# Kernel tuning notes

Measured on AMD Instinct MI355X. Metric: run time of the kernel, lower is better.

## Reference

```python
import jax, jax.numpy as jnp
import numpy as np


def setup_inputs() -> dict:
    key = jax.random.key(0)
    ks = jax.random.split(key, 6)
    B, H, N, C, O, G = 4, 24, 512, 120, 512, 5
    x = jax.random.normal(ks[0], (B, H, N, C), dtype=jnp.float32)
    t_indices = jnp.arange(H, dtype=jnp.int64)
    time_emb = jax.random.normal(ks[1], (H, 8), dtype=jnp.float32)
    # kaiming-uniform-ish init for base linear weight
    fan_in = C + 8
    bound = float(np.sqrt(6.0 / fan_in))
    base_w = jax.random.uniform(ks[2], (O, C + 8), minval=-bound, maxval=bound, dtype=jnp.float32)
    base_b = jax.random.uniform(ks[3], (O,), minval=-1.0 / np.sqrt(fan_in), maxval=1.0 / np.sqrt(fan_in), dtype=jnp.float32)
    spline_weight = jax.random.uniform(ks[4], (O, C + 8, G), minval=-0.1, maxval=0.1, dtype=jnp.float32)
    return {"x": x, "t_indices": t_indices, "time_emb": time_emb,
            "base_w": base_w, "base_b": base_b, "spline_weight": spline_weight}


def reference(x, t_indices, time_emb, base_w, base_b, spline_weight):
    B, H, N, C = x.shape
    G = spline_weight.shape[-1]
    grid = jnp.linspace(-1.0, 1.0, G, dtype=x.dtype)  # non-trainable buffer
    # time embedding lookup, broadcast over batch and nodes: [B,H,N,8]
    t_emb = jnp.broadcast_to(time_emb[t_indices][None, :, None, :], (B, H, N, time_emb.shape[-1]))
    x_in = jnp.concatenate([x, t_emb], axis=-1)  # [B,H,N,C+8]
    # base path: SiLU then linear
    base = jnp.einsum('bhni,oi->bhno', jax.nn.silu(x_in), base_w) + base_b
    # RBF basis: [B,H,N,C+8,G]
    inv_h = (G - 1) / 2.0  # 1 / (2/(G-1))
    basis = jnp.exp(-(((x_in[..., None] - grid) * inv_h) ** 2))
    spline = jnp.einsum('bhnig,oig->bhno', basis, spline_weight)
    return base + spline
```

## Files before the change

### kernel.cpp

```cpp
#include <hip/hip_runtime.h>
#include <hip/hip_bf16.h>

typedef __attribute__((ext_vector_type(4))) float f32x4;
typedef __attribute__((ext_vector_type(8))) short bf16x8;

#define GLDS16(gp, lp) __builtin_amdgcn_global_load_lds( \
    (__attribute__((address_space(1))) void*)(void*)(gp), \
    (__attribute__((address_space(3))) void*)(lp), 16, 0, 0)

static constexpr int Mtot = 49152;
static constexpr int Otot = 512;
static constexpr int Hh   = 24;

__device__ inline unsigned short f2bf(float f) {
    __hip_bfloat16 h = __float2bfloat16(f);
    unsigned short u;
    __builtin_memcpy(&u, &h, 2);
    return u;
}

__global__ __launch_bounds__(256) void prep_W(
        const float* __restrict__ bw, const float* __restrict__ sw,
        uint4* __restrict__ Wt)
{
    int tid = blockIdx.x * 256 + threadIdx.x;
    int p    = tid & 15;
    int o    = (tid >> 4) & 511;
    int iter = tid >> 13;
    int ck = p ^ (o & 7);
    unsigned u[4] = {0u, 0u, 0u, 0u};
    if (ck < 12) {
        unsigned short s[8];
        #pragma unroll
        for (int e = 0; e < 8; ++e) {
            int k = iter * 96 + ck * 8 + e;
            int i = k / 6, f = k - i * 6;
            float v = (f == 0) ? bw[o * 128 + i] : sw[(o * 128 + i) * 5 + (f - 1)];
            s[e] = f2bf(v);
        }
        #pragma unroll
        for (int n = 0; n < 4; ++n) u[n] = s[2 * n] | ((unsigned)s[2 * n + 1] << 16);
    }
    Wt[tid] = make_uint4(u[0], u[1], u[2], u[3]);
}

__global__ __launch_bounds__(256, 2) void gemm_kan(
        const float* __restrict__ x, const int* __restrict__ t_idx,
        const float* __restrict__ temb,
        const char* __restrict__ Wt,
        const float* __restrict__ bias,
        float* __restrict__ out)
{
    __shared__ char AsB[64 * 256];
    __shared__ char BsB[256 * 256];
    const int t    = threadIdx.x;
    const int wave = t >> 6;
    const int lane = t & 63;
    const int ll   = lane & 15;
    const int q4   = lane >> 4;
    const int wn   = wave * 64;
    const int m_base = blockIdx.y * 64;
    const int n_base = blockIdx.x * 256;

    f32x4 acc[4][4] = {};

    const char* bsrc0 = Wt + (size_t)(n_base + wn) * 256 + lane * 16;
    char* ldsB = BsB + wn * 256;

    const int row = t >> 2;
    const int q   = t & 3;
    const int ht  = t_idx[(m_base >> 9) % Hh];
    const float* xrow = x + (size_t)(m_base + row) * 120;
    const float* trow = temb + ht * 8;

    auto chanptr = [&](int i0) -> const float* {
        return (i0 < 120) ? (xrow + i0) : (trow + (i0 - 120));
    };

    float4 xv = *(const float4*)chanptr(4 * q);

    constexpr float C1 = 0.36787944117f;
    constexpr float C4 = 0.01831563889f;

    #pragma unroll
    for (int it = 0; it < 8; ++it) {
        const char* bsrc = bsrc0 + (size_t)it * (512 * 256);
        #pragma unroll
        for (int p = 0; p < 16; ++p)
            GLDS16(bsrc + p * 1024, ldsB + p * 1024);

        const float4 cur = xv;
        if (it < 7) xv = *(const float4*)chanptr((it + 1) * 16 + 4 * q);

        float v[4] = {cur.x, cur.y, cur.z, cur.w};
        unsigned short s[24];
        #pragma unroll
        for (int c = 0; c < 4; ++c) {
            const float vv = v[c];
            s[c * 6 + 0] = f2bf(vv * __builtin_amdgcn_rcpf(1.0f + __expf(-vv)));
            const float tt = __expf(-4.0f * vv * vv);
            const float uu = __expf(4.0f * vv);
            const float rr = __builtin_amdgcn_rcpf(uu);
            const float tu = tt * uu, tr = tt * rr;
            s[c * 6 + 1] = f2bf(tr * rr * C4);
            s[c * 6 + 2] = f2bf(tr * C1);
            s[c * 6 + 3] = f2bf(tt);
            s[c * 6 + 4] = f2bf(tu * C1);
            s[c * 6 + 5] = f2bf(tu * uu * C4);
        }
        #pragma unroll
        for (int j = 0; j < 3; ++j) {
            const int ck = 3 * q + j;
            const int phys = ck ^ (row & 7);
            unsigned u[4];
            #pragma unroll
            for (int n = 0; n < 4; ++n)
                u[n] = s[j * 8 + 2 * n] | ((unsigned)s[j * 8 + 2 * n + 1] << 16);
            *(uint4*)(AsB + row * 256 + phys * 16) = make_uint4(u[0], u[1], u[2], u[3]);
        }
        __syncthreads();

        #pragma unroll
        for (int kk = 0; kk < 3; ++kk) {
            bf16x8 af[4], bf[4];
            #pragma unroll
            for (int mi = 0; mi < 4; ++mi) {
                const int r = mi * 16 + ll;
                af[mi] = *(const bf16x8*)(AsB + r * 256 + (((kk * 4 + q4) ^ (ll & 7)) * 16));
            }
            #pragma unroll
            for (int ni = 0; ni < 4; ++ni) {
                const int r = wn + ni * 16 + ll;
                bf[ni] = *(const bf16x8*)(BsB + r * 256 + (((kk * 4 + q4) ^ (ll & 7)) * 16));
            }
            #pragma unroll
            for (int mi = 0; mi < 4; ++mi)
                #pragma unroll
                for (int ni = 0; ni < 4; ++ni)
                    acc[mi][ni] = __builtin_amdgcn_mfma_f32_16x16x32_bf16(
                        af[mi], bf[ni], acc[mi][ni], 0, 0, 0);
        }
        __syncthreads();
    }

    const int col0 = n_base + wn + ll;
    const int row0 = m_base + q4 * 4;
    #pragma unroll
    for (int ni = 0; ni < 4; ++ni) {
        const int col = col0 + ni * 16;
        const float bv = bias[col];
        #pragma unroll
        for (int mi = 0; mi < 4; ++mi) {
            #pragma unroll
            for (int r = 0; r < 4; ++r) {
                out[(long)(row0 + mi * 16 + r) * Otot + col] = acc[mi][ni][r] + bv;
            }
        }
    }
}

extern "C" void kernel_launch(void* const* d_in, const int* in_sizes, int n_in,
                              void* d_out, int out_size, void* d_ws, size_t ws_size,
                              hipStream_t stream) {
    const float* x    = (const float*)d_in[0];
    const int*   tidx = (const int*)  d_in[1];
    const float* temb = (const float*)d_in[2];
    const float* bw   = (const float*)d_in[3];
    const float* bb   = (const float*)d_in[4];
    const float* sw   = (const float*)d_in[5];
    float* out = (float*)d_out;

    char* Wt = (char*)d_ws;

    prep_W<<<65536 / 256, 256, 0, stream>>>(bw, sw, (uint4*)Wt);
    gemm_kan<<<dim3(Otot / 256, Mtot / 64), 256, 0, stream>>>(
        x, tidx, temb, Wt, bb, out);
}
```

Before: 171.1 us.

## Retile KAN GEMM to 128x128 blocks with chunk-major LDS and block swizzle

Changes the block tile from 64x256 to 128x128 with a 2x2 wave layout, so each block computes twice as many A-side basis rows and shares them across fewer B columns. The LDS layout becomes chunk-major (16-byte chunk by row) with no XOR swizzle, and the prepacked weights are laid out the same way, which also drops the padding chunks. LDS use falls from 80KB to 48KB, allowing 3 blocks per CU, and a grouped blockIdx swizzle is meant to improve L2 reuse. The aim is to cut redundant activation/basis computation and weight traffic per output. The risk is LDS bank conflicts from the unswizzled layout.

```diff
diff --git a/kernel.cpp b/kernel.cpp
--- a/kernel.cpp
+++ b/kernel.cpp
@@ -23,52 +23,51 @@
         const float* __restrict__ bw, const float* __restrict__ sw,
         uint4* __restrict__ Wt)
 {
-    int tid = blockIdx.x * 256 + threadIdx.x;
-    int p    = tid & 15;
-    int o    = (tid >> 4) & 511;
-    int iter = tid >> 13;
-    int ck = p ^ (o & 7);
-    unsigned u[4] = {0u, 0u, 0u, 0u};
-    if (ck < 12) {
-        unsigned short s[8];
-        #pragma unroll
-        for (int e = 0; e < 8; ++e) {
-            int k = iter * 96 + ck * 8 + e;
-            int i = k / 6, f = k - i * 6;
-            float v = (f == 0) ? bw[o * 128 + i] : sw[(o * 128 + i) * 5 + (f - 1)];
-            s[e] = f2bf(v);
-        }
-        #pragma unroll
-        for (int n = 0; n < 4; ++n) u[n] = s[2 * n] | ((unsigned)s[2 * n + 1] << 16);
+    const int tid = blockIdx.x * 256 + threadIdx.x;
+    const int col = tid & 511;
+    const int cc  = tid >> 9;
+    const int k0  = cc * 8;
+    unsigned short s[8];
+    #pragma unroll
+    for (int e = 0; e < 8; ++e) {
+        const int k = k0 + e;
+        const int i = k / 6, f = k - i * 6;
+        const float v = (f == 0) ? bw[col * 128 + i]
+                                 : sw[(col * 128 + i) * 5 + (f - 1)];
+        s[e] = f2bf(v);
     }
-    Wt[tid] = make_uint4(u[0], u[1], u[2], u[3]);
+    uint4 u;
+    u.x = s[0] | ((unsigned)s[1] << 16);
+    u.y = s[2] | ((unsigned)s[3] << 16);
+    u.z = s[4] | ((unsigned)s[5] << 16);
+    u.w = s[6] | ((unsigned)s[7] << 16);
+    Wt[tid] = u;
 }
 
-__global__ __launch_bounds__(256, 2) void gemm_kan(
+__global__ __launch_bounds__(256, 3) void gemm_kan(
         const float* __restrict__ x, const int* __restrict__ t_idx,
         const float* __restrict__ temb,
         const char* __restrict__ Wt,
         const float* __restrict__ bias,
         float* __restrict__ out)
 {
-    __shared__ char AsB[64 * 256];
-    __shared__ char BsB[256 * 256];
+    __shared__ char Alds[12 * 128 * 16];
+    __shared__ char Blds[12 * 128 * 16];
     const int t    = threadIdx.x;
     const int wave = t >> 6;
     const int lane = t & 63;
     const int ll   = lane & 15;
     const int q4   = lane >> 4;
-    const int wn   = wave * 64;
-    const int m_base = blockIdx.y * 64;
-    const int n_base = blockIdx.x * 256;
+    const int wm   = (wave >> 1) * 64;
+    const int wn   = (wave & 1) * 64;
 
-    f32x4 acc[4][4] = {};
+    const int bid = blockIdx.x;
+    const int swz = (bid & 7) * 192 + (bid >> 3);
+    const int m_base = (swz >> 2) * 128;
+    const int n_base = (swz & 3) * 128;
 
-    const char* bsrc0 = Wt + (size_t)(n_base + wn) * 256 + lane * 16;
-    char* ldsB = BsB + wn * 256;
-
-    const int row = t >> 2;
-    const int q   = t & 3;
+    const int row = t >> 1;
+    const int hh  = t & 1;
     const int ht  = t_idx[(m_base >> 9) % Hh];
     const float* xrow = x + (size_t)(m_base + row) * 120;
     const float* trow = temb + ht * 8;
@@ -77,25 +76,40 @@
         return (i0 < 120) ? (xrow + i0) : (trow + (i0 - 120));
     };
 
-    float4 xv = *(const float4*)chanptr(4 * q);
+    f32x4 acc[4][4] = {};
+
+    float4 xa, xb;
+    {
+        const float* p = chanptr(hh * 8);
+        xa = *(const float4*)p;
+        xb = *(const float4*)(p + 4);
+    }
 
     constexpr float C1 = 0.36787944117f;
     constexpr float C4 = 0.01831563889f;
 
     #pragma unroll
     for (int it = 0; it < 8; ++it) {
-        const char* bsrc = bsrc0 + (size_t)it * (512 * 256);
         #pragma unroll
-        for (int p = 0; p < 16; ++p)
-            GLDS16(bsrc + p * 1024, ldsB + p * 1024);
+        for (int j = 0; j < 6; ++j) {
+            const int c = wave * 3 + (j >> 1);
+            const int g = (j & 1) * 64;
+            const char* src = Wt + (((size_t)(it * 12 + c) * 512 + n_base + g) << 4)
+                              + lane * 16;
+            GLDS16(src, Blds + ((c * 128 + g) << 4));
+        }
 
-        const float4 cur = xv;
-        if (it < 7) xv = *(const float4*)chanptr((it + 1) * 16 + 4 * q);
+        const float4 ca = xa, cb = xb;
+        if (it < 7) {
+            const float* p = chanptr((it + 1) * 16 + hh * 8);
+            xa = *(const float4*)p;
+            xb = *(const float4*)(p + 4);
+        }
 
-        float v[4] = {cur.x, cur.y, cur.z, cur.w};
-        unsigned short s[24];
+        const float v[8] = {ca.x, ca.y, ca.z, ca.w, cb.x, cb.y, cb.z, cb.w};
+        unsigned short s[48];
         #pragma unroll
-        for (int c = 0; c < 4; ++c) {
+        for (int c = 0; c < 8; ++c) {
             const float vv = v[c];
             s[c * 6 + 0] = f2bf(vv * __builtin_amdgcn_rcpf(1.0f + __expf(-vv)));
             const float tt = __expf(-4.0f * vv * vv);
@@ -109,30 +123,26 @@
             s[c * 6 + 5] = f2bf(tu * uu * C4);
         }
         #pragma unroll
-        for (int j = 0; j < 3; ++j) {
-            const int ck = 3 * q + j;
-            const int phys = ck ^ (row & 7);
+        for (int j = 0; j < 6; ++j) {
+            const int ck = 6 * hh + j;
             unsigned u[4];
             #pragma unroll
             for (int n = 0; n < 4; ++n)
                 u[n] = s[j * 8 + 2 * n] | ((unsigned)s[j * 8 + 2 * n + 1] << 16);
-            *(uint4*)(AsB + row * 256 + phys * 16) = make_uint4(u[0], u[1], u[2], u[3]);
+            *(uint4*)(Alds + ((ck * 128 + row) << 4)) = make_uint4(u[0], u[1], u[2], u[3]);
         }
         __syncthreads();
 
         #pragma unroll
         for (int kk = 0; kk < 3; ++kk) {
+            const int ch = kk * 4 + q4;
             bf16x8 af[4], bf[4];
             #pragma unroll
-            for (int mi = 0; mi < 4; ++mi) {
-                const int r = mi * 16 + ll;
-                af[mi] = *(const bf16x8*)(AsB + r * 256 + (((kk * 4 + q4) ^ (ll & 7)) * 16));
-            }
+            for (int mi = 0; mi < 4; ++mi)
+                af[mi] = *(const bf16x8*)(Alds + ((ch * 128 + wm + mi * 16 + ll) << 4));
             #pragma unroll
-            for (int ni = 0; ni < 4; ++ni) {
-                const int r = wn + ni * 16 + ll;
-                bf[ni] = *(const bf16x8*)(BsB + r * 256 + (((kk * 4 + q4) ^ (ll & 7)) * 16));
-            }
+            for (int ni = 0; ni < 4; ++ni)
+                bf[ni] = *(const bf16x8*)(Blds + ((ch * 128 + wn + ni * 16 + ll) << 4));
             #pragma unroll
             for (int mi = 0; mi < 4; ++mi)
                 #pragma unroll
@@ -144,7 +154,7 @@
     }
 
     const int col0 = n_base + wn + ll;
-    const int row0 = m_base + q4 * 4;
+    const int row0 = m_base + wm + q4 * 4;
     #pragma unroll
     for (int ni = 0; ni < 4; ++ni) {
         const int col = col0 + ni * 16;
@@ -172,7 +182,6 @@
 
     char* Wt = (char*)d_ws;
 
-    prep_W<<<65536 / 256, 256, 0, stream>>>(bw, sw, (uint4*)Wt);
-    gemm_kan<<<dim3(Otot / 256, Mtot / 64), 256, 0, stream>>>(
-        x, tidx, temb, Wt, bb, out);
+    prep_W<<<49152 / 256, 256, 0, stream>>>(bw, sw, (uint4*)Wt);
+    gemm_kan<<<1536, 256, 0, stream>>>(x, tidx, temb, Wt, bb, out);
 }
```

Measured after the change: 167.6 us. 1.02x faster.
